# Optimization experiments

Measured on AMD Instinct MI355X. Metric: run time of the kernel, lower is better.

Reference implementation:

```python
import jax, jax.numpy as jnp
import numpy as np

B, S1, S2 = 1024, 25, 10          # batch, hop-1 fanout, hop-2 fanout
N, D, H, C = 100000, 256, 128, 64  # n_node, in_dim, per-branch out_dim, n_class


def setup_inputs() -> dict:
    key = jax.random.key(0)
    ks = jax.random.split(key, 10)
    rn = lambda k, shape: jax.random.normal(k, shape, dtype=jnp.float32) * 0.05
    return {
        "ids0": jax.random.randint(ks[0], (B,), 0, N),
        "ids1": jax.random.randint(ks[1], (B * S1,), 0, N),
        "ids2": jax.random.randint(ks[2], (B * S1 * S2,), 0, N),
        "features": jax.random.normal(ks[3], (N, D), dtype=jnp.float32),
        # aggregator layer 1 (in D, out 2H after concat)
        "Wx1": rn(ks[4], (D, H)), "bx1": jnp.zeros((H,), jnp.float32),
        "Wn1": rn(ks[5], (D, H)), "bn1": jnp.zeros((H,), jnp.float32),
        # aggregator layer 2 (in 2H, out 2H)
        "Wx2": rn(ks[6], (2 * H, H)), "bx2": jnp.zeros((H,), jnp.float32),
        "Wn2": rn(ks[7], (2 * H, H)), "bn2": jnp.zeros((H,), jnp.float32),
        # final linear head
        "Wfc": rn(ks[8], (2 * H, C)), "bfc": jnp.zeros((C,), jnp.float32),
    }


def _mean_agg(x, neibs, Wx, bx, Wn, bn, act):
    # neibs: [x_rows * fanout, d] -> mean over fanout, then concat of two linears
    n = neibs.reshape(x.shape[0], -1, neibs.shape[-1]).mean(axis=1)
    out = jnp.concatenate([x @ Wx + bx, n @ Wn + bn], axis=-1)
    return act(out)


def reference(ids0, ids1, ids2, features,
              Wx1, bx1, Wn1, bn1, Wx2, bx2, Wn2, bn2, Wfc, bfc):
    # hop-wise feature gathers (identity prep)
    h0 = features[ids0]   # [B, D]
    h1 = features[ids1]   # [B*S1, D]
    h2 = features[ids2]   # [B*S1*S2, D]
    # layer 1 aggregation (relu), applied to consecutive hop pairs
    g0 = _mean_agg(h0, h1, Wx1, bx1, Wn1, bn1, jax.nn.relu)   # [B, 2H]
    g1 = _mean_agg(h1, h2, Wx1, bx1, Wn1, bn1, jax.nn.relu)   # [B*S1, 2H]
    # layer 2 aggregation (identity activation on last layer)
    f0 = _mean_agg(g0, g1, Wx2, bx2, Wn2, bn2, lambda v: v)   # [B, 2H]
    return f0 @ Wfc + bfc  # [B, C]
```

## Files before the change

### kernel.cpp

```cpp
#include <hip/hip_runtime.h>

#define DD 256
#define HH 128
#define CC 64
#define BB 1024
#define SS1 25
#define SS2 10
#define NN 100000

typedef __attribute__((ext_vector_type(8))) short bf16x8;
typedef __attribute__((ext_vector_type(4))) float f32x4;

__device__ inline unsigned short f2b(float x) {
    union { float f; unsigned u; } v; v.f = x;
    unsigned r = (v.u + 0x7fffu + ((v.u >> 16) & 1u)) >> 16;
    return (unsigned short)r;
}
__device__ inline float b2f(unsigned u16) {
    union { unsigned u; float f; } v; v.u = u16 << 16;
    return v.f;
}

__global__ __launch_bounds__(256)
void prep_w(const float* __restrict__ Wx, const float* __restrict__ Wn,
            unsigned short* __restrict__ Wsw) {
    const int t    = blockIdx.x * 256 + threadIdx.x;
    const int lane = t & 63;
    const int frag = t >> 6;
    const int kc = frag >> 4, nt = frag & 15;
    const int quad = lane >> 4, lr = lane & 15;
    unsigned short v[8];
#pragma unroll
    for (int j = 0; j < 8; ++j) {
        int k = kc * 32 + quad * 8 + j;
        int n = nt * 16 + lr;
        float w = (n < HH) ? Wx[k * HH + n] : Wn[k * HH + (n - HH)];
        v[j] = f2b(w);
    }
    ((uint4*)Wsw)[t] = *(uint4*)v;
}

#define PQ_BLOCKS 512
#define PQ_TILES  (NN / 32)
#define AS 264

#define PQ_ISSUE(VREG, TIDX)                                                  \
    {                                                                         \
        const float* fn_ = feat + (long)(TIDX) * 32 * DD + sc * 8;            \
        _Pragma("unroll")                                                     \
        for (int i_ = 0; i_ < 4; ++i_) {                                      \
            const float4* s_ = (const float4*)(fn_ + (long)(i_ * 8 + srow) * DD); \
            VREG[2 * i_]     = s_[0];                                         \
            VREG[2 * i_ + 1] = s_[1];                                         \
        }                                                                     \
    }

#define PQ_STEP(VREG)                                                         \
    {                                                                         \
              \
        _Pragma("unroll")                                                     \
        for (int i_ = 0; i_ < 4; ++i_) {                                      \
            int row_ = i_ * 8 + srow;                                         \
            float4 a_ = VREG[2 * i_], b_ = VREG[2 * i_ + 1];                  \
            unsigned short w8_[8] = { f2b(a_.x), f2b(a_.y), f2b(a_.z), f2b(a_.w), \
                                      f2b(b_.x), f2b(b_.y), f2b(b_.z), f2b(b_.w) }; \
            *(uint4*)&sAO[0][row_ * AS + sc * 8] = *(uint4*)w8_;              \
        }                                                                     \
                                \
        {                                                                     \
            long t2_ = tile + 2L * PQ_BLOCKS;                                 \
            if (t2_ < PQ_TILES) PQ_ISSUE(VREG, t2_);                          \
        }                                                                     \
                       \
        asm volatile("s_waitcnt lgkmcnt(0)" ::: "memory");                    \
        __builtin_amdgcn_s_barrier();                                         \
                                          \
        f32x4 acc[2][4] = {};                                                 \
        _Pragma("unroll")                                                     \
        for (int kc = 0; kc < 8; ++kc) {                                      \
            bf16x8 a0 = *(const bf16x8*)&sAO[0][(lr)      * AS + kc * 32 + quad * 8]; \
            bf16x8 a1 = *(const bf16x8*)&sAO[0][(16 + lr) * AS + kc * 32 + quad * 8]; \
            _Pragma("unroll")                                                 \
            for (int j = 0; j < 4; ++j) {                                     \
                acc[0][j] = __builtin_amdgcn_mfma_f32_16x16x32_bf16(a0, B[kc][j], acc[0][j], 0, 0, 0); \
                acc[1][j] = __builtin_amdgcn_mfma_f32_16x16x32_bf16(a1, B[kc][j], acc[1][j], 0, 0, 0); \
            }                                                                 \
        }                                                                     \
                  \
        _Pragma("unroll")                                                     \
        for (int rt = 0; rt < 2; ++rt)                                        \
            _Pragma("unroll")                                                 \
            for (int j = 0; j < 4; ++j) {                                     \
                int col_ = (w * 4 + j) * 16 + lr;                             \
                _Pragma("unroll")                                             \
                for (int r = 0; r < 4; ++r)                                   \
                    sAO[1][(rt * 16 + quad * 4 + r) * AS + col_] = f2b(acc[rt][j][r]); \
            }                                                                 \
                  \
        asm volatile("s_waitcnt lgkmcnt(0)" ::: "memory");                    \
        __builtin_amdgcn_s_barrier();                                         \
                                           \
        _Pragma("unroll")                                                     \
        for (int i_ = 0; i_ < 4; ++i_) {                                      \
            int id_  = i_ * 256 + t;                                          \
            int row_ = id_ >> 5, ch_ = id_ & 31;                              \
            uint4 d_ = *(uint4*)&sAO[1][row_ * AS + ch_ * 8];                 \
            *(uint4*)&PQb[((long)tile * 32 + row_) * DD + ch_ * 8] = d_;      \
        }                                                                     \
    }

__global__ __launch_bounds__(256, 2)
void pq_gemm(const float* __restrict__ feat,
             const unsigned short* __restrict__ Wsw,
             unsigned short* __restrict__ PQb) {
    __shared__ unsigned short sAO[2][32 * AS];
    const int t    = threadIdx.x;
    const int w    = t >> 6, lane = t & 63;
    const int quad = lane >> 4, lr = lane & 15;

    bf16x8 B[8][4];
#pragma unroll
    for (int kc = 0; kc < 8; ++kc)
#pragma unroll
        for (int j = 0; j < 4; ++j)
            B[kc][j] = *(const bf16x8*)&Wsw[((kc * 16 + (w * 4 + j)) * 64 + lane) * 8];

    const int srow = t >> 5, sc = t & 31;

    float4 va[8], vb[8];
    long tile = blockIdx.x;
    PQ_ISSUE(va, tile);
    if (tile + PQ_BLOCKS < PQ_TILES) PQ_ISSUE(vb, tile + PQ_BLOCKS);

    while (true) {
        PQ_STEP(va);
        tile += PQ_BLOCKS; if (tile >= PQ_TILES) break;
        PQ_STEP(vb);
        tile += PQ_BLOCKS; if (tile >= PQ_TILES) break;
    }
}

__global__ __launch_bounds__(512)
void megatail(const unsigned short* __restrict__ PQb,
              const int* __restrict__ ids0, const int* __restrict__ ids1,
              const int* __restrict__ ids2,
              const float* __restrict__ bx1, const float* __restrict__ bn1,
              const float* __restrict__ Wx2, const float* __restrict__ bx2,
              const float* __restrict__ Wn2, const float* __restrict__ bn2,
              const float* __restrict__ Wfc, const float* __restrict__ bfc,
              float* __restrict__ out) {
    __shared__ float sred[16][3 * HH];
    __shared__ float g0L[DD];
    __shared__ float gmL[DD];
    __shared__ float FP[2][DD];
    __shared__ float FL[DD];
    __shared__ float sp[8][CC];
    const int i    = blockIdx.x;
    const int t    = threadIdx.x;
    const int wv   = t >> 6, lane = t & 63;
    const int sub  = lane >> 5, lr = lane & 31;
    const int slot = wv * 2 + sub;

    const float4 bx = *(const float4*)&bx1[lr * 4];
    const float4 bn = *(const float4*)&bn1[lr * 4];
    float4 xs  = {0.f, 0.f, 0.f, 0.f};
    float4 ns  = {0.f, 0.f, 0.f, 0.f};
    float4 g0n = {0.f, 0.f, 0.f, 0.f};

#pragma unroll
    for (int it = 0; it < 2; ++it) {
        int s = slot + it * 16;
        if (s < SS1) {
            int row  = i * SS1 + s;
            long xr  = (long)ids1[row];
            uint2 xv  = *(const uint2*)&PQb[xr * DD + lr * 4];
            uint2 nv0 = *(const uint2*)&PQb[xr * DD + HH + lr * 4];
            int myid = ids2[row * SS2 + (lr % SS2)];
            float4 acc = {0.f, 0.f, 0.f, 0.f};
#pragma unroll
            for (int j = 0; j < SS2; ++j) {
                long nr = (long)__shfl(myid, (lane & 32) + j);
                uint2 nv = *(const uint2*)&PQb[nr * DD + HH + lr * 4];
                acc.x += b2f(nv.x & 0xffff); acc.y += b2f(nv.x >> 16);
                acc.z += b2f(nv.y & 0xffff); acc.w += b2f(nv.y >> 16);
            }
            constexpr float inv2 = 1.f / SS2;
            xs.x += fmaxf(b2f(xv.x & 0xffff) + bx.x, 0.f);
            xs.y += fmaxf(b2f(xv.x >> 16)    + bx.y, 0.f);
            xs.z += fmaxf(b2f(xv.y & 0xffff) + bx.z, 0.f);
            xs.w += fmaxf(b2f(xv.y >> 16)    + bx.w, 0.f);
            ns.x += fmaxf(acc.x * inv2 + bn.x, 0.f);
            ns.y += fmaxf(acc.y * inv2 + bn.y, 0.f);
            ns.z += fmaxf(acc.z * inv2 + bn.z, 0.f);
            ns.w += fmaxf(acc.w * inv2 + bn.w, 0.f);
            g0n.x += b2f(nv0.x & 0xffff); g0n.y += b2f(nv0.x >> 16);
            g0n.z += b2f(nv0.y & 0xffff); g0n.w += b2f(nv0.y >> 16);
        }
    }
    *(float4*)&sred[slot][lr * 4]          = xs;
    *(float4*)&sred[slot][HH + lr * 4]     = ns;
    *(float4*)&sred[slot][2 * HH + lr * 4] = g0n;
    __syncthreads();

    if (t < 256) {
        float r = 0.f;
#pragma unroll
        for (int k = 0; k < 16; ++k) r += sred[k][t];
        gmL[t] = r * (1.f / SS1);
    } else {
        const int c = t - 256;
        float v;
        if (c < HH) {
            unsigned short u = PQb[(long)ids0[i] * DD + c];
            v = fmaxf(b2f(u) + bx1[c], 0.f);
        } else {
            float s2 = 0.f;
#pragma unroll
            for (int k = 0; k < 16; ++k) s2 += sred[k][2 * HH + (c - HH)];
            v = fmaxf(s2 * (1.f / SS1) + bn1[c - HH], 0.f);
        }
        g0L[c] = v;
    }
    __syncthreads();

    {
        const int c = t & 255, h = t >> 8;
        const bool xhalf = (c < HH);
        const float* __restrict__ W    = xhalf ? Wx2 : Wn2;
        const float* __restrict__ srcL = xhalf ? g0L : gmL;
        const int cc = c & (HH - 1);
        float fa = 0.f;
#pragma unroll 8
        for (int k = h * 128; k < h * 128 + 128; ++k) fa += srcL[k] * W[k * HH + cc];
        FP[h][c] = fa;
    }
    __syncthreads();
    if (t < 256)
        FL[t] = FP[0][t] + FP[1][t] + ((t < HH) ? bx2[t] : bn2[t - HH]);
    __syncthreads();

    {
        const int col = t & (CC - 1), q = t >> 6;
        float p = 0.f;
#pragma unroll 8
        for (int k = q * 32; k < q * 32 + 32; ++k) p += FL[k] * Wfc[k * CC + col];
        sp[q][col] = p;
    }
    __syncthreads();
    if (t < CC) {
        float r = bfc[t];
#pragma unroll
        for (int q = 0; q < 8; ++q) r += sp[q][t];
        out[(long)i * CC + t] = r;
    }
}

extern "C" void kernel_launch(void* const* d_in, const int* in_sizes, int n_in,
                              void* d_out, int out_size, void* d_ws, size_t ws_size,
                              hipStream_t stream) {
    const int*   ids0 = (const int*)d_in[0];
    const int*   ids1 = (const int*)d_in[1];
    const int*   ids2 = (const int*)d_in[2];
    const float* feat = (const float*)d_in[3];
    const float* Wx1  = (const float*)d_in[4];
    const float* bx1  = (const float*)d_in[5];
    const float* Wn1  = (const float*)d_in[6];
    const float* bn1  = (const float*)d_in[7];
    const float* Wx2  = (const float*)d_in[8];
    const float* bx2  = (const float*)d_in[9];
    const float* Wn2  = (const float*)d_in[10];
    const float* bn2  = (const float*)d_in[11];
    const float* Wfc  = (const float*)d_in[12];
    const float* bfc  = (const float*)d_in[13];
    float* out = (float*)d_out;

    unsigned short* PQb = (unsigned short*)d_ws;
    unsigned short* Wsw = PQb + (long)NN * DD;

    prep_w<<<32, 256, 0, stream>>>(Wx1, Wn1, Wsw);
    pq_gemm<<<PQ_BLOCKS, 256, 0, stream>>>(feat, Wsw, PQb);
    megatail<<<BB, 512, 0, stream>>>(PQb, ids0, ids1, ids2, bx1, bn1,
                                     Wx2, bx2, Wn2, bn2, Wfc, bfc, out);
}
```

Baseline: 217.0 us.

## Use 16-lane groups with 16-byte gathers and wavefront shuffle reduction in megatail

```diff
diff --git a/kernel.cpp b/kernel.cpp
--- a/kernel.cpp
+++ b/kernel.cpp
@@ -149,7 +149,7 @@
               const float* __restrict__ Wn2, const float* __restrict__ bn2,
               const float* __restrict__ Wfc, const float* __restrict__ bfc,
               float* __restrict__ out) {
-    __shared__ float sred[16][3 * HH];
+    __shared__ float sred[8][3 * HH];
     __shared__ float g0L[DD];
     __shared__ float gmL[DD];
     __shared__ float FP[2][DD];
@@ -158,68 +158,89 @@
     const int i    = blockIdx.x;
     const int t    = threadIdx.x;
     const int wv   = t >> 6, lane = t & 63;
-    const int sub  = lane >> 5, lr = lane & 31;
-    const int slot = wv * 2 + sub;
-
-    const float4 bx = *(const float4*)&bx1[lr * 4];
-    const float4 bn = *(const float4*)&bn1[lr * 4];
-    float4 xs  = {0.f, 0.f, 0.f, 0.f};
-    float4 ns  = {0.f, 0.f, 0.f, 0.f};
-    float4 g0n = {0.f, 0.f, 0.f, 0.f};
-
-#pragma unroll
-    for (int it = 0; it < 2; ++it) {
-        int s = slot + it * 16;
-        if (s < SS1) {
-            int row  = i * SS1 + s;
-            long xr  = (long)ids1[row];
-            uint2 xv  = *(const uint2*)&PQb[xr * DD + lr * 4];
-            uint2 nv0 = *(const uint2*)&PQb[xr * DD + HH + lr * 4];
-            int myid = ids2[row * SS2 + (lr % SS2)];
-            float4 acc = {0.f, 0.f, 0.f, 0.f};
-#pragma unroll
-            for (int j = 0; j < SS2; ++j) {
-                long nr = (long)__shfl(myid, (lane & 32) + j);
-                uint2 nv = *(const uint2*)&PQb[nr * DD + HH + lr * 4];
-                acc.x += b2f(nv.x & 0xffff); acc.y += b2f(nv.x >> 16);
-                acc.z += b2f(nv.y & 0xffff); acc.w += b2f(nv.y >> 16);
-            }
-            constexpr float inv2 = 1.f / SS2;
-            xs.x += fmaxf(b2f(xv.x & 0xffff) + bx.x, 0.f);
-            xs.y += fmaxf(b2f(xv.x >> 16)    + bx.y, 0.f);
-            xs.z += fmaxf(b2f(xv.y & 0xffff) + bx.z, 0.f);
-            xs.w += fmaxf(b2f(xv.y >> 16)    + bx.w, 0.f);
-            ns.x += fmaxf(acc.x * inv2 + bn.x, 0.f);
-            ns.y += fmaxf(acc.y * inv2 + bn.y, 0.f);
-            ns.z += fmaxf(acc.z * inv2 + bn.z, 0.f);
-            ns.w += fmaxf(acc.w * inv2 + bn.w, 0.f);
-            g0n.x += b2f(nv0.x & 0xffff); g0n.y += b2f(nv0.x >> 16);
-            g0n.z += b2f(nv0.y & 0xffff); g0n.w += b2f(nv0.y >> 16);
+    const int l16  = lane & 15;
+    const int slot = wv * 4 + (lane >> 4);
+    const int c0   = l16 * 8;
+
+    float xs[8], ns[8], g0n[8];
+#pragma unroll
+    for (int k = 0; k < 8; ++k) { xs[k] = 0.f; ns[k] = 0.f; g0n[k] = 0.f; }
+
+    if (slot < SS1) {
+        const int row = i * SS1 + slot;
+        const long xr = (long)ids1[row];
+        uint4 xv  = *(const uint4*)&PQb[xr * DD + c0];
+        uint4 nv0 = *(const uint4*)&PQb[xr * DD + HH + c0];
+        int myid = ids2[row * SS2 + (l16 % SS2)];
+        float pa[8];
+#pragma unroll
+        for (int k = 0; k < 8; ++k) pa[k] = 0.f;
+#pragma unroll
+        for (int j = 0; j < SS2; ++j) {
+            long nr = (long)__shfl(myid, (lane & 48) + j);
+            uint4 nv = *(const uint4*)&PQb[nr * DD + HH + c0];
+            pa[0] += b2f(nv.x & 0xffff); pa[1] += b2f(nv.x >> 16);
+            pa[2] += b2f(nv.y & 0xffff); pa[3] += b2f(nv.y >> 16);
+            pa[4] += b2f(nv.z & 0xffff); pa[5] += b2f(nv.z >> 16);
+            pa[6] += b2f(nv.w & 0xffff); pa[7] += b2f(nv.w >> 16);
         }
-    }
-    *(float4*)&sred[slot][lr * 4]          = xs;
-    *(float4*)&sred[slot][HH + lr * 4]     = ns;
-    *(float4*)&sred[slot][2 * HH + lr * 4] = g0n;
-    __syncthreads();
-
-    if (t < 256) {
+        const float4 bxa = *(const float4*)&bx1[c0];
+        const float4 bxb = *(const float4*)&bx1[c0 + 4];
+        const float4 bna = *(const float4*)&bn1[c0];
+        const float4 bnb = *(const float4*)&bn1[c0 + 4];
+        constexpr float inv2 = 1.f / SS2;
+        xs[0] = fmaxf(b2f(xv.x & 0xffff) + bxa.x, 0.f);
+        xs[1] = fmaxf(b2f(xv.x >> 16)    + bxa.y, 0.f);
+        xs[2] = fmaxf(b2f(xv.y & 0xffff) + bxa.z, 0.f);
+        xs[3] = fmaxf(b2f(xv.y >> 16)    + bxa.w, 0.f);
+        xs[4] = fmaxf(b2f(xv.z & 0xffff) + bxb.x, 0.f);
+        xs[5] = fmaxf(b2f(xv.z >> 16)    + bxb.y, 0.f);
+        xs[6] = fmaxf(b2f(xv.w & 0xffff) + bxb.z, 0.f);
+        xs[7] = fmaxf(b2f(xv.w >> 16)    + bxb.w, 0.f);
+        ns[0] = fmaxf(pa[0] * inv2 + bna.x, 0.f);
+        ns[1] = fmaxf(pa[1] * inv2 + bna.y, 0.f);
+        ns[2] = fmaxf(pa[2] * inv2 + bna.z, 0.f);
+        ns[3] = fmaxf(pa[3] * inv2 + bna.w, 0.f);
+        ns[4] = fmaxf(pa[4] * inv2 + bnb.x, 0.f);
+        ns[5] = fmaxf(pa[5] * inv2 + bnb.y, 0.f);
+        ns[6] = fmaxf(pa[6] * inv2 + bnb.z, 0.f);
+        ns[7] = fmaxf(pa[7] * inv2 + bnb.w, 0.f);
+        g0n[0] = b2f(nv0.x & 0xffff); g0n[1] = b2f(nv0.x >> 16);
+        g0n[2] = b2f(nv0.y & 0xffff); g0n[3] = b2f(nv0.y >> 16);
+        g0n[4] = b2f(nv0.z & 0xffff); g0n[5] = b2f(nv0.z >> 16);
+        g0n[6] = b2f(nv0.w & 0xffff); g0n[7] = b2f(nv0.w >> 16);
+    }
+
+#pragma unroll
+    for (int k = 0; k < 8; ++k) {
+        xs[k]  += __shfl_xor(xs[k], 16);  xs[k]  += __shfl_xor(xs[k], 32);
+        ns[k]  += __shfl_xor(ns[k], 16);  ns[k]  += __shfl_xor(ns[k], 32);
+        g0n[k] += __shfl_xor(g0n[k], 16); g0n[k] += __shfl_xor(g0n[k], 32);
+    }
+    if (lane < 16) {
+        *(float4*)&sred[wv][c0]              = make_float4(xs[0], xs[1], xs[2], xs[3]);
+        *(float4*)&sred[wv][c0 + 4]          = make_float4(xs[4], xs[5], xs[6], xs[7]);
+        *(float4*)&sred[wv][HH + c0]         = make_float4(ns[0], ns[1], ns[2], ns[3]);
+        *(float4*)&sred[wv][HH + c0 + 4]     = make_float4(ns[4], ns[5], ns[6], ns[7]);
+        *(float4*)&sred[wv][2 * HH + c0]     = make_float4(g0n[0], g0n[1], g0n[2], g0n[3]);
+        *(float4*)&sred[wv][2 * HH + c0 + 4] = make_float4(g0n[4], g0n[5], g0n[6], g0n[7]);
+    }
+    __syncthreads();
+
+    if (t < 384) {
         float r = 0.f;
 #pragma unroll
-        for (int k = 0; k < 16; ++k) r += sred[k][t];
-        gmL[t] = r * (1.f / SS1);
+        for (int k = 0; k < 8; ++k) r += sred[k][t];
+        if (t < 256) {
+            gmL[t] = r * (1.f / SS1);
+        } else {
+            const int c = t - 256;
+            g0L[HH + c] = fmaxf(r * (1.f / SS1) + bn1[c], 0.f);
+        }
     } else {
-        const int c = t - 256;
-        float v;
-        if (c < HH) {
-            unsigned short u = PQb[(long)ids0[i] * DD + c];
-            v = fmaxf(b2f(u) + bx1[c], 0.f);
-        } else {
-            float s2 = 0.f;
-#pragma unroll
-            for (int k = 0; k < 16; ++k) s2 += sred[k][2 * HH + (c - HH)];
-            v = fmaxf(s2 * (1.f / SS1) + bn1[c - HH], 0.f);
-        }
-        g0L[c] = v;
+        const int c = t - 384;
+        unsigned short u = PQb[(long)ids0[i] * DD + c];
+        g0L[c] = fmaxf(b2f(u) + bx1[c], 0.f);
     }
     __syncthreads();
 
```

Result: no change. 219.0 us (+0.9%).
